# Performance work log

Measured on AMD Instinct MI355X. Metric: run time of the kernel, lower is better.

## Reference

```python
import jax, jax.numpy as jnp
import numpy as np

E = 512        # embed_dim
H = 16         # num_heads
R = 8          # num_relation_heads
NH = H - R     # num_normal_heads
HD = E // H    # head_dim
SCALING = HD ** -0.5
B, LQ, LK = 2, 2048, 2048


def setup_inputs() -> dict:
    key = jax.random.key(0)
    ks = jax.random.split(key, 14)
    s = 1.0 / np.sqrt(E)  # keep pre-softmax logits moderate so exp() is stable
    inp = {
        "query": jax.random.normal(ks[0], (B, LQ, E), jnp.float32),
        "key": jax.random.normal(ks[1], (B, LK, E), jnp.float32),
        "value": jax.random.normal(ks[2], (B, LK, E), jnp.float32),
        "relation_weights": jax.random.uniform(ks[3], (B, R, LQ, LK), jnp.float32),
        "Wq": jax.random.normal(ks[4], (E, E), jnp.float32) * s,
        "bq": jnp.zeros((E,), jnp.float32),
        "Wk": jax.random.normal(ks[5], (E, E), jnp.float32) * s,
        "bk": jnp.zeros((E,), jnp.float32),
        "Wv": jax.random.normal(ks[6], (E, E), jnp.float32) * s,
        "bv": jnp.zeros((E,), jnp.float32),
        "Wo": jax.random.normal(ks[7], (E, E), jnp.float32) * s,
        "bo": jnp.zeros((E,), jnp.float32),
        "ln_gamma": jnp.ones((E,), jnp.float32),
        "ln_beta": jnp.zeros((E,), jnp.float32),
    }
    return inp


def reference(query, key, value, relation_weights, Wq, bq, Wk, bk, Wv, bv, Wo, bo, ln_gamma, ln_beta):
    b, lq, _ = query.shape
    lk = key.shape[1]
    # projections; weights stored as [in, out] so y = x @ W + b
    q = (query @ Wq + bq).reshape(b, lq, H, HD)
    k = (key @ Wk + bk).reshape(b, lk, H, HD)
    v = (value @ Wv + bv).reshape(b, lk, H, HD)
    # scores: [B, H, Lq, Lk]
    scores = jnp.einsum("bqhd,bkhd->bhqk", q, k) * SCALING
    # normal heads: standard softmax
    normal_attn = jax.nn.softmax(scores[:, :NH], axis=-1)
    # relation heads: exp(scores) * relation_weights, renormalized
    rel = jnp.exp(scores[:, NH:]) * relation_weights
    rel = rel / (rel.sum(axis=-1, keepdims=True) + 1e-6)
    attn = jnp.concatenate([normal_attn, rel], axis=1)  # [B, H, Lq, Lk]
    # weighted values -> [B, Lq, E]
    out = jnp.einsum("bhqk,bkhd->bqhd", attn, v).reshape(b, lq, E)
    out = out @ Wo + bo
    # LayerNorm (eps=1e-5, torch default)
    mu = out.mean(axis=-1, keepdims=True)
    var = out.var(axis=-1, keepdims=True)
    out = (out - mu) * jax.lax.rsqrt(var + 1e-5) * ln_gamma + ln_beta
    return out
```

## Files before the change

kernel.cpp:

```cpp
#include <hip/hip_runtime.h>


using u16 = unsigned short;
using u32 = unsigned int;

typedef __attribute__((ext_vector_type(8))) short bf16x8;
typedef __attribute__((ext_vector_type(4))) float f32x4;

#define H_  16
#define NH_ 8
#define HD_ 32
#define L_  2048
#define E_  512
#define B_  2
#define M_  4096
#define KSPLIT 2
static constexpr float SCALE_ = 0.1767766952966369f;

__device__ inline u16 f2bf(float x) {
  union { float f; u32 u; } v; v.f = x;
  u32 r = v.u + 0x7FFFu + ((v.u >> 16) & 1u);
  return (u16)(r >> 16);
}
__device__ inline float bf2f(u16 x) {
  union { u32 u; float f; } v; v.u = ((u32)x) << 16; return v.f;
}
__device__ inline u16 f2h(float x) {
  union { _Float16 h; u16 u; } v; v.h = (_Float16)x; return v.u;
}
__device__ inline float h2f(u16 x) {
  union { u16 u; _Float16 h; } v; v.u = x; return (float)v.h;
}

__global__ __launch_bounds__(256) void k_cvt3(const float* __restrict__ a, const float* __restrict__ b,
                                              const float* __restrict__ c,
                                              u16* __restrict__ oa, u16* __restrict__ ob, u16* __restrict__ oc) {
  int w = blockIdx.y;
  const float* s = (w == 0) ? a : (w == 1) ? b : c;
  u16* d = (w == 0) ? oa : (w == 1) ? ob : oc;
  size_t i = ((size_t)blockIdx.x * 256 + threadIdx.x) * 4;
  float4 v = *(const float4*)(s + i);
  uint2 pk;
  pk.x = (u32)f2bf(v.x) | ((u32)f2bf(v.y) << 16);
  pk.y = (u32)f2bf(v.z) | ((u32)f2bf(v.w) << 16);
  *(uint2*)(d + i) = pk;
}

__global__ __launch_bounds__(256) void k_wtrans(const float* __restrict__ Wq, const float* __restrict__ Wk,
                                                const float* __restrict__ Wv, const float* __restrict__ Wo,
                                                u16* __restrict__ Tq, u16* __restrict__ Tk,
                                                u16* __restrict__ Tv, u16* __restrict__ To) {
  int z = blockIdx.z;
  const float* W = (z == 0) ? Wq : (z == 1) ? Wk : (z == 2) ? Wv : Wo;
  u16* T = (z == 0) ? Tq : (z == 1) ? Tk : (z == 2) ? Tv : To;
  __shared__ u16 tile[64][65];
  int r0 = blockIdx.y * 64, c0 = blockIdx.x * 64;
  int tw = threadIdx.x >> 6, tl = threadIdx.x & 63;
#pragma unroll
  for (int i = 0; i < 16; ++i) {
    int r = i * 4 + tw;
    tile[r][tl] = f2bf(W[(size_t)(r0 + r) * E_ + c0 + tl]);
  }
  __syncthreads();
#pragma unroll
  for (int i = 0; i < 16; ++i) {
    int r = i * 4 + tw;
    T[(size_t)(c0 + r) * E_ + r0 + tl] = tile[tl][r];
  }
}

template <int MODE>
__device__ inline void gemm_body(const u16* __restrict__ A, const u16* __restrict__ Bt,
                                 const float* __restrict__ bias, void* __restrict__ out) {
  __shared__ __align__(16) u16 smem[2 * 128 * 72];
  u16* As = smem;
  u16* Bs = smem + 128 * 72;
  const int tid = threadIdx.x;
  const int lane = tid & 63, wid = tid >> 6;
  const int m0 = blockIdx.x * 128, n0 = blockIdx.y * 128;
  const int wm = (wid >> 1) * 64, wn = (wid & 1) * 64;
  const int mrow = lane & 15, quad = lane >> 4;
  f32x4 acc[4][4] = {};
  for (int k0 = 0; k0 < 512; k0 += 64) {
    __syncthreads();
#pragma unroll
    for (int i = 0; i < 4; ++i) {
      int task = i * 256 + tid;
      int r = task >> 3, c = task & 7;
      *(uint4*)(As + r * 72 + c * 8) = *(const uint4*)(A + (size_t)(m0 + r) * 512 + k0 + c * 8);
      *(uint4*)(Bs + r * 72 + c * 8) = *(const uint4*)(Bt + (size_t)(n0 + r) * 512 + k0 + c * 8);
    }
    __syncthreads();
#pragma unroll
    for (int kk = 0; kk < 64; kk += 32) {
      bf16x8 af[4], bfr[4];
#pragma unroll
      for (int f = 0; f < 4; ++f)
        af[f] = *(const bf16x8*)(As + (wm + f * 16 + mrow) * 72 + kk + quad * 8);
#pragma unroll
      for (int f = 0; f < 4; ++f)
        bfr[f] = *(const bf16x8*)(Bs + (wn + f * 16 + mrow) * 72 + kk + quad * 8);
#pragma unroll
      for (int fm = 0; fm < 4; ++fm)
#pragma unroll
        for (int fn = 0; fn < 4; ++fn)
          acc[fm][fn] = __builtin_amdgcn_mfma_f32_16x16x32_bf16(af[fm], bfr[fn], acc[fm][fn], 0, 0, 0);
    }
  }
  if (MODE == 0) {
    __syncthreads();
    u16* wscr = smem + wid * (64 * 72);
#pragma unroll
    for (int fn = 0; fn < 4; ++fn) {
      float bv = bias[n0 + wn + fn * 16 + mrow];
#pragma unroll
      for (int fm = 0; fm < 4; ++fm)
#pragma unroll
        for (int r = 0; r < 4; ++r)
          wscr[(fm * 16 + quad * 4 + r) * 72 + fn * 16 + mrow] = f2bf(acc[fm][fn][r] + bv);
    }
    asm volatile("s_waitcnt lgkmcnt(0)" ::: "memory");
    const int hg0 = (n0 + wn) >> 5;
#pragma unroll
    for (int c = 0; c < 8; ++c) {
      int linear = c * 64 + lane;
      int hh = linear >> 8;
      int rem = linear & 255;
      int lm = rem >> 2, j = rem & 3;
      uint4 vv = *(const uint4*)(wscr + lm * 72 + hh * 32 + j * 8);
      int gm = m0 + wm + lm;
      int bb = gm >> 11, q = gm & (L_ - 1);
      *(uint4*)((u16*)out + (((size_t)(bb * H_ + hg0 + hh)) * L_ + q) * HD_ + j * 8) = vv;
    }
  } else {
#pragma unroll
    for (int fn = 0; fn < 4; ++fn) {
      int gn = n0 + wn + fn * 16 + mrow;
      float bv = bias[gn];
#pragma unroll
      for (int fm = 0; fm < 4; ++fm)
#pragma unroll
        for (int r = 0; r < 4; ++r) {
          int gm = m0 + wm + fm * 16 + quad * 4 + r;
          ((float*)out)[(size_t)gm * E_ + gn] = acc[fm][fn][r] + bv;
        }
    }
  }
}

__global__ __launch_bounds__(256) void k_gemm_qkv(const u16* Xq, const u16* Xk, const u16* Xv,
                                                  const u16* Tq, const u16* Tk, const u16* Tv,
                                                  const float* bq, const float* bk, const float* bv,
                                                  u16* Qb, u16* Kb, u16* Vb) {
  int z = blockIdx.z;
  const u16* A = (z == 0) ? Xq : (z == 1) ? Xk : Xv;
  const u16* T = (z == 0) ? Tq : (z == 1) ? Tk : Tv;
  const float* bi = (z == 0) ? bq : (z == 1) ? bk : bv;
  u16* o = (z == 0) ? Qb : (z == 1) ? Kb : Vb;
  gemm_body<0>(A, T, bi, o);
}

__global__ __launch_bounds__(256) void k_gemm_o(const u16* A, const u16* T, const float* bi, float* Y) {
  gemm_body<1>(A, T, bi, Y);
}

__global__ __launch_bounds__(256) void k_attn(const u16* __restrict__ Qb, const u16* __restrict__ Kb,
                                              const u16* __restrict__ Vb, const float* __restrict__ relw,
                                              u16* __restrict__ Pnum, float* __restrict__ Pden) {
  const int tid = threadIdx.x, lane = tid & 63, wid = tid >> 6;
  const int q0 = blockIdx.x * 64;
  const int h = blockIdx.y;
  const int b = blockIdx.z & (B_ - 1), s = blockIdx.z >> 1;
  const int kbase = s * (L_ / KSPLIT);
  const bool isrel = (h >= NH_);
  const size_t headOff = ((size_t)(b * H_ + h)) * L_ * HD_;
  const float* wbase = isrel ? relw + ((size_t)(b * (H_ - NH_) + (h - NH_))) * L_ * L_ : nullptr;

  __shared__ __align__(16) u16 Qs[64 * 40];
  __shared__ __align__(16) u16 Ks[64 * 40];
  __shared__ __align__(16) u16 Vts[32 * 72];
  __shared__ __align__(16) u16 Ps[4][16 * 72];
  __shared__ __align__(16) u16 Ws[64 * 68];

  {
    int r = tid >> 2, c = tid & 3;
    *(uint4*)(Qs + r * 40 + c * 8) = *(const uint4*)(Qb + headOff + (size_t)(q0 + r) * HD_ + c * 8);
  }
  __syncthreads();
  const int mrow = lane & 15, quad = lane >> 4;
  bf16x8 qa = *(const bf16x8*)(Qs + (wid * 16 + mrow) * 40 + quad * 8);
  f32x4 accd[2] = {};
  float den[4] = {0.f, 0.f, 0.f, 0.f};

  for (int kt = kbase; kt < kbase + L_ / KSPLIT; kt += 64) {
    __syncthreads();
    if (tid < 128) {
      int p = tid >> 2, c = tid & 3;
      const u16* vsrc = Vb + headOff + (size_t)(kt + 2 * p) * HD_ + c * 8;
      uint4 v0 = *(const uint4*)(vsrc);
      uint4 v1 = *(const uint4*)(vsrc + HD_);
      const u16* s0 = (const u16*)&v0;
      const u16* s1 = (const u16*)&v1;
#pragma unroll
      for (int i = 0; i < 8; ++i) {
        u32 pk = (u32)s0[i] | ((u32)s1[i] << 16);
        *(u32*)(Vts + (c * 8 + i) * 72 + 2 * p) = pk;
      }
    } else {
      int t2 = tid - 128;
#pragma unroll
      for (int i = 0; i < 2; ++i) {
        int task = t2 * 2 + i;
        int r = task >> 2, c = task & 3;
        *(uint4*)(Ks + r * 40 + c * 8) = *(const uint4*)(Kb + headOff + (size_t)(kt + r) * HD_ + c * 8);
      }
    }
    if (isrel) {
      int q = tid >> 2, kc = (tid & 3) * 4;
      const float* wsrc = wbase + (size_t)(q0 + q) * L_ + kt + kc;
#pragma unroll
      for (int j = 0; j < 4; ++j) {
        float4 w4 = *(const float4*)(wsrc + j * 16);
        uint2 pk;
        pk.x = (u32)f2bf(w4.x) | ((u32)f2bf(w4.y) << 16);
        pk.y = (u32)f2bf(w4.z) | ((u32)f2bf(w4.w) << 16);
        *(uint2*)(Ws + q * 68 + kc + j * 16) = pk;
      }
    }
    __syncthreads();

    u16* pw = Ps[wid];
#pragma unroll
    for (int f = 0; f < 4; ++f) {
      bf16x8 kb = *(const bf16x8*)(Ks + (f * 16 + mrow) * 40 + quad * 8);
      f32x4 z = {0.f, 0.f, 0.f, 0.f};
      f32x4 sc = __builtin_amdgcn_mfma_f32_16x16x32_bf16(qa, kb, z, 0, 0, 0);
#pragma unroll
      for (int r = 0; r < 4; ++r) {
        float e = __expf(sc[r] * SCALE_);
        if (isrel)
          e *= bf2f(Ws[(wid * 16 + quad * 4 + r) * 68 + f * 16 + mrow]);
        den[r] += e;
        pw[(quad * 4 + r) * 72 + f * 16 + mrow] = f2bf(e);
      }
    }
    asm volatile("s_waitcnt lgkmcnt(0)" ::: "memory");
#pragma unroll
    for (int kk = 0; kk < 2; ++kk) {
      bf16x8 pa = *(const bf16x8*)(pw + mrow * 72 + kk * 32 + quad * 8);
#pragma unroll
      for (int dh = 0; dh < 2; ++dh) {
        bf16x8 vbf = *(const bf16x8*)(Vts + (dh * 16 + mrow) * 72 + kk * 32 + quad * 8);
        accd[dh] = __builtin_amdgcn_mfma_f32_16x16x32_bf16(pa, vbf, accd[dh], 0, 0, 0);
      }
    }
  }

#pragma unroll
  for (int off = 1; off < 16; off <<= 1)
#pragma unroll
    for (int r = 0; r < 4; ++r) den[r] += __shfl_xor(den[r], off, 64);

  const size_t pidx = ((size_t)(s * B_ + b) * H_ + h) * L_;
#pragma unroll
  for (int dh = 0; dh < 2; ++dh)
#pragma unroll
    for (int r = 0; r < 4; ++r) {
      int qg = q0 + wid * 16 + quad * 4 + r;
      Pnum[(pidx + qg) * HD_ + dh * 16 + mrow] = f2h(accd[dh][r]);
    }
  if (mrow == 0) {
    int qg = q0 + wid * 16 + quad * 4;
    float4 dv = {den[0], den[1], den[2], den[3]};
    *(float4*)(Pden + pidx + qg) = dv;
  }
}

__global__ __launch_bounds__(256) void k_combine(const u16* __restrict__ Pnum, const float* __restrict__ Pden,
                                                 u16* __restrict__ AO) {
  int row = blockIdx.x;
  int tid = threadIdx.x;
  int b = row >> 11, q = row & (L_ - 1);
  int e0 = tid * 2;
  int h = e0 >> 5, d = e0 & (HD_ - 1);
  size_t i0 = ((size_t)(0 * B_ + b) * H_ + h) * L_ + q;
  size_t i1 = ((size_t)(1 * B_ + b) * H_ + h) * L_ + q;
  u32 n0 = *(const u32*)(Pnum + i0 * HD_ + d);
  u32 n1 = *(const u32*)(Pnum + i1 * HD_ + d);
  float den = Pden[i0] + Pden[i1] + ((h >= NH_) ? 1e-6f : 0.f);
  float rinv = 1.0f / den;
  float x = (h2f((u16)n0) + h2f((u16)n1)) * rinv;
  float y = (h2f((u16)(n0 >> 16)) + h2f((u16)(n1 >> 16))) * rinv;
  u32 pk = (u32)f2bf(x) | ((u32)f2bf(y) << 16);
  *(u32*)(AO + (size_t)row * E_ + e0) = pk;
}

__global__ __launch_bounds__(256) void k_ln(const float* __restrict__ Y, const float* __restrict__ gamma,
                                            const float* __restrict__ beta, float* __restrict__ out) {
  int row = blockIdx.x, tid = threadIdx.x;
  const float* y = Y + (size_t)row * E_;
  float2 v = *(const float2*)(y + tid * 2);
  float s = v.x + v.y, sq = v.x * v.x + v.y * v.y;
#pragma unroll
  for (int off = 1; off < 64; off <<= 1) {
    s += __shfl_xor(s, off, 64);
    sq += __shfl_xor(sq, off, 64);
  }
  __shared__ float ss[4], ssq[4];
  int wid = tid >> 6, lane = tid & 63;
  if (lane == 0) { ss[wid] = s; ssq[wid] = sq; }
  __syncthreads();
  s = ss[0] + ss[1] + ss[2] + ss[3];
  sq = ssq[0] + ssq[1] + ssq[2] + ssq[3];
  float mean = s * (1.f / E_);
  float var = sq * (1.f / E_) - mean * mean;
  float rstd = rsqrtf(var + 1e-5f);
  float2 g = *(const float2*)(gamma + tid * 2);
  float2 be = *(const float2*)(beta + tid * 2);
  float2 o;
  o.x = (v.x - mean) * rstd * g.x + be.x;
  o.y = (v.y - mean) * rstd * g.y + be.y;
  *(float2*)(out + (size_t)row * E_ + tid * 2) = o;
}

extern "C" void kernel_launch(void* const* d_in, const int* in_sizes, int n_in,
                              void* d_out, int out_size, void* d_ws, size_t ws_size,
                              hipStream_t stream) {
  const float* query = (const float*)d_in[0];
  const float* key   = (const float*)d_in[1];
  const float* value = (const float*)d_in[2];
  const float* relw  = (const float*)d_in[3];
  const float* Wq = (const float*)d_in[4];
  const float* bq = (const float*)d_in[5];
  const float* Wk = (const float*)d_in[6];
  const float* bk = (const float*)d_in[7];
  const float* Wv = (const float*)d_in[8];
  const float* bv = (const float*)d_in[9];
  const float* Wo = (const float*)d_in[10];
  const float* bo = (const float*)d_in[11];
  const float* gamma = (const float*)d_in[12];
  const float* beta  = (const float*)d_in[13];

  char* ws = (char*)d_ws;
  u16* Xq = (u16*)(ws + 0);
  u16* Xk = (u16*)(ws + 4194304);
  u16* Xv = (u16*)(ws + 8388608);
  u16* Tq = (u16*)(ws + 12582912);
  u16* Tk = (u16*)(ws + 13107200);
  u16* Tv = (u16*)(ws + 13631488);
  u16* To = (u16*)(ws + 14155776);
  u16* Qb = (u16*)(ws + 14680064);
  u16* Kb = (u16*)(ws + 18874368);
  u16* Vb = (u16*)(ws + 23068672);
  u16* AO = (u16*)(ws + 27262976);
  u16*   Pnum = (u16*)(ws + 0);
  float* Pden = (float*)(ws + 8388608);
  float* Y = (float*)(ws + 0);

  k_cvt3<<<dim3(2048, 3, 1), 256, 0, stream>>>(query, key, value, Xq, Xk, Xv);
  k_wtrans<<<dim3(8, 8, 4), 256, 0, stream>>>(Wq, Wk, Wv, Wo, Tq, Tk, Tv, To);
  k_gemm_qkv<<<dim3(32, 4, 3), 256, 0, stream>>>(Xq, Xk, Xv, Tq, Tk, Tv, bq, bk, bv, Qb, Kb, Vb);
  k_attn<<<dim3(32, 16, B_ * KSPLIT), 256, 0, stream>>>(Qb, Kb, Vb, relw, Pnum, Pden);
  k_combine<<<M_, 256, 0, stream>>>(Pnum, Pden, AO);
  k_gemm_o<<<dim3(32, 4, 1), 256, 0, stream>>>(AO, To, bo, Y);
  k_ln<<<M_, 256, 0, stream>>>(Y, gamma, beta, (float*)d_out);
}
```

Before: 498.3 us.

## Fuse prep kernels and combine into GEMM, prefetch attention tiles, use fp16 PV

The input conversion and weight transpose become one launch, and the split-K combine moves into the output GEMM's A-tile load, dropping a kernel and the AO round trip. The attention loop now register-prefetches the next K, V and relation-weight tile while the current one is computed. Softmax scale and log2(e) are folded into Q at projection time so the loop uses exp2. P and V are stored as fp16 and use the f16 MFMA. These cut launches, global traffic and memory latency, at the cost of more registers and possible fp16 range or precision issues.

```diff
diff --git a/kernel.cpp b/kernel.cpp
--- a/kernel.cpp
+++ b/kernel.cpp
@@ -5,6 +5,7 @@
 using u32 = unsigned int;
 
 typedef __attribute__((ext_vector_type(8))) short bf16x8;
+typedef __attribute__((ext_vector_type(8))) _Float16 f16x8;
 typedef __attribute__((ext_vector_type(4))) float f32x4;
 
 #define H_  16
@@ -15,7 +16,7 @@
 #define B_  2
 #define M_  4096
 #define KSPLIT 2
-static constexpr float SCALE_ = 0.1767766952966369f;
+static constexpr float QSCALE_ = 0.17677669529663689f * 1.44269504088896340f;
 
 __device__ inline u16 f2bf(float x) {
   union { float f; u32 u; } v; v.f = x;
@@ -32,29 +33,32 @@
   union { u16 u; _Float16 h; } v; v.u = x; return (float)v.h;
 }
 
-__global__ __launch_bounds__(256) void k_cvt3(const float* __restrict__ a, const float* __restrict__ b,
-                                              const float* __restrict__ c,
-                                              u16* __restrict__ oa, u16* __restrict__ ob, u16* __restrict__ oc) {
-  int w = blockIdx.y;
-  const float* s = (w == 0) ? a : (w == 1) ? b : c;
-  u16* d = (w == 0) ? oa : (w == 1) ? ob : oc;
-  size_t i = ((size_t)blockIdx.x * 256 + threadIdx.x) * 4;
-  float4 v = *(const float4*)(s + i);
-  uint2 pk;
-  pk.x = (u32)f2bf(v.x) | ((u32)f2bf(v.y) << 16);
-  pk.y = (u32)f2bf(v.z) | ((u32)f2bf(v.w) << 16);
-  *(uint2*)(d + i) = pk;
-}
-
-__global__ __launch_bounds__(256) void k_wtrans(const float* __restrict__ Wq, const float* __restrict__ Wk,
-                                                const float* __restrict__ Wv, const float* __restrict__ Wo,
-                                                u16* __restrict__ Tq, u16* __restrict__ Tk,
-                                                u16* __restrict__ Tv, u16* __restrict__ To) {
-  int z = blockIdx.z;
+__global__ __launch_bounds__(256) void k_prep(const float* __restrict__ qa, const float* __restrict__ ka,
+                                              const float* __restrict__ va,
+                                              u16* __restrict__ oq, u16* __restrict__ ok, u16* __restrict__ ov,
+                                              const float* __restrict__ Wq, const float* __restrict__ Wk,
+                                              const float* __restrict__ Wv, const float* __restrict__ Wo,
+                                              u16* __restrict__ Tq, u16* __restrict__ Tk,
+                                              u16* __restrict__ Tv, u16* __restrict__ To) {
+  __shared__ u16 tile[64][65];
+  int y = blockIdx.y;
+  if (y < 3) {
+    const float* s = (y == 0) ? qa : (y == 1) ? ka : va;
+    u16* d = (y == 0) ? oq : (y == 1) ? ok : ov;
+    size_t i = ((size_t)blockIdx.x * 256 + threadIdx.x) * 4;
+    float4 v = *(const float4*)(s + i);
+    uint2 pk;
+    pk.x = (u32)f2bf(v.x) | ((u32)f2bf(v.y) << 16);
+    pk.y = (u32)f2bf(v.z) | ((u32)f2bf(v.w) << 16);
+    *(uint2*)(d + i) = pk;
+    return;
+  }
+  if (blockIdx.x >= 256) return;
+  int bid = blockIdx.x;
+  int z = bid >> 6, rem = bid & 63;
+  int r0 = ((rem >> 3) & 7) * 64, c0 = (rem & 7) * 64;
   const float* W = (z == 0) ? Wq : (z == 1) ? Wk : (z == 2) ? Wv : Wo;
   u16* T = (z == 0) ? Tq : (z == 1) ? Tk : (z == 2) ? Tv : To;
-  __shared__ u16 tile[64][65];
-  int r0 = blockIdx.y * 64, c0 = blockIdx.x * 64;
   int tw = threadIdx.x >> 6, tl = threadIdx.x & 63;
 #pragma unroll
   for (int i = 0; i < 16; ++i) {
@@ -71,7 +75,8 @@
 
 template <int MODE>
 __device__ inline void gemm_body(const u16* __restrict__ A, const u16* __restrict__ Bt,
-                                 const float* __restrict__ bias, void* __restrict__ out) {
+                                 const float* __restrict__ bias, void* __restrict__ out,
+                                 const float* __restrict__ pden, float oscale, int ofmt) {
   __shared__ __align__(16) u16 smem[2 * 128 * 72];
   u16* As = smem;
   u16* Bs = smem + 128 * 72;
@@ -87,8 +92,27 @@
     for (int i = 0; i < 4; ++i) {
       int task = i * 256 + tid;
       int r = task >> 3, c = task & 7;
-      *(uint4*)(As + r * 72 + c * 8) = *(const uint4*)(A + (size_t)(m0 + r) * 512 + k0 + c * 8);
       *(uint4*)(Bs + r * 72 + c * 8) = *(const uint4*)(Bt + (size_t)(n0 + r) * 512 + k0 + c * 8);
+      if (MODE == 0) {
+        *(uint4*)(As + r * 72 + c * 8) = *(const uint4*)(A + (size_t)(m0 + r) * 512 + k0 + c * 8);
+      } else {
+        int gm = m0 + r;
+        int bb = gm >> 11, q = gm & (L_ - 1);
+        int e0 = k0 + c * 8;
+        int hh = e0 >> 5, d = e0 & (HD_ - 1);
+        size_t i0 = ((size_t)(0 * B_ + bb) * H_ + hh) * L_ + q;
+        size_t i1 = ((size_t)(1 * B_ + bb) * H_ + hh) * L_ + q;
+        uint4 n0v = *(const uint4*)(A + i0 * HD_ + d);
+        uint4 n1v = *(const uint4*)(A + i1 * HD_ + d);
+        float den = pden[i0] + pden[i1] + ((hh >= NH_) ? 1e-6f : 0.f);
+        float rinv = __builtin_amdgcn_rcpf(den);
+        const u16* p0 = (const u16*)&n0v;
+        const u16* p1 = (const u16*)&n1v;
+        u16 o8[8];
+#pragma unroll
+        for (int j = 0; j < 8; ++j) o8[j] = f2bf((h2f(p0[j]) + h2f(p1[j])) * rinv);
+        *(uint4*)(As + r * 72 + c * 8) = *(const uint4*)o8;
+      }
     }
     __syncthreads();
 #pragma unroll
@@ -116,8 +140,10 @@
 #pragma unroll
       for (int fm = 0; fm < 4; ++fm)
 #pragma unroll
-        for (int r = 0; r < 4; ++r)
-          wscr[(fm * 16 + quad * 4 + r) * 72 + fn * 16 + mrow] = f2bf(acc[fm][fn][r] + bv);
+        for (int r = 0; r < 4; ++r) {
+          float x = (acc[fm][fn][r] + bv) * oscale;
+          wscr[(fm * 16 + quad * 4 + r) * 72 + fn * 16 + mrow] = ofmt ? f2h(x) : f2bf(x);
+        }
     }
     asm volatile("s_waitcnt lgkmcnt(0)" ::: "memory");
     const int hg0 = (n0 + wn) >> 5;
@@ -157,11 +183,14 @@
   const u16* T = (z == 0) ? Tq : (z == 1) ? Tk : Tv;
   const float* bi = (z == 0) ? bq : (z == 1) ? bk : bv;
   u16* o = (z == 0) ? Qb : (z == 1) ? Kb : Vb;
-  gemm_body<0>(A, T, bi, o);
-}
-
-__global__ __launch_bounds__(256) void k_gemm_o(const u16* A, const u16* T, const float* bi, float* Y) {
-  gemm_body<1>(A, T, bi, Y);
+  float os = (z == 0) ? QSCALE_ : 1.0f;
+  int of = (z == 2) ? 1 : 0;
+  gemm_body<0>(A, T, bi, o, nullptr, os, of);
+}
+
+__global__ __launch_bounds__(256) void k_gemm_o(const u16* Pnum, const u16* T, const float* bi,
+                                                float* Y, const float* Pden) {
+  gemm_body<1>(Pnum, T, bi, Y, Pden, 1.0f, 0);
 }
 
 __global__ __launch_bounds__(256) void k_attn(const u16* __restrict__ Qb, const u16* __restrict__ Kb,
@@ -172,6 +201,7 @@
   const int h = blockIdx.y;
   const int b = blockIdx.z & (B_ - 1), s = blockIdx.z >> 1;
   const int kbase = s * (L_ / KSPLIT);
+  const int kend = kbase + L_ / KSPLIT;
   const bool isrel = (h >= NH_);
   const size_t headOff = ((size_t)(b * H_ + h)) * L_ * HD_;
   const float* wbase = isrel ? relw + ((size_t)(b * (H_ - NH_) + (h - NH_))) * L_ * L_ : nullptr;
@@ -192,41 +222,58 @@
   f32x4 accd[2] = {};
   float den[4] = {0.f, 0.f, 0.f, 0.f};
 
-  for (int kt = kbase; kt < kbase + L_ / KSPLIT; kt += 64) {
-    __syncthreads();
+  uint4 rA, rB;
+  float4 rw[4];
+  const int vp = tid >> 2, vc = tid & 3;
+  const int t2 = tid - 128;
+  const int wq = tid >> 2, wkc = (tid & 3) * 4;
+
+  auto LOAD = [&](int kt) {
     if (tid < 128) {
-      int p = tid >> 2, c = tid & 3;
-      const u16* vsrc = Vb + headOff + (size_t)(kt + 2 * p) * HD_ + c * 8;
-      uint4 v0 = *(const uint4*)(vsrc);
-      uint4 v1 = *(const uint4*)(vsrc + HD_);
-      const u16* s0 = (const u16*)&v0;
-      const u16* s1 = (const u16*)&v1;
+      const u16* vsrc = Vb + headOff + (size_t)(kt + 2 * vp) * HD_ + vc * 8;
+      rA = *(const uint4*)(vsrc);
+      rB = *(const uint4*)(vsrc + HD_);
+    } else {
+      int task0 = t2 * 2, task1 = t2 * 2 + 1;
+      rA = *(const uint4*)(Kb + headOff + (size_t)(kt + (task0 >> 2)) * HD_ + (task0 & 3) * 8);
+      rB = *(const uint4*)(Kb + headOff + (size_t)(kt + (task1 >> 2)) * HD_ + (task1 & 3) * 8);
+    }
+    if (isrel) {
+      const float* wsrc = wbase + (size_t)(q0 + wq) * L_ + kt + wkc;
+#pragma unroll
+      for (int j = 0; j < 4; ++j) rw[j] = *(const float4*)(wsrc + j * 16);
+    }
+  };
+  auto WRITE = [&]() {
+    if (tid < 128) {
+      const u16* s0 = (const u16*)&rA;
+      const u16* s1 = (const u16*)&rB;
 #pragma unroll
       for (int i = 0; i < 8; ++i) {
         u32 pk = (u32)s0[i] | ((u32)s1[i] << 16);
-        *(u32*)(Vts + (c * 8 + i) * 72 + 2 * p) = pk;
+        *(u32*)(Vts + (vc * 8 + i) * 72 + 2 * vp) = pk;
       }
     } else {
-      int t2 = tid - 128;
-#pragma unroll
-      for (int i = 0; i < 2; ++i) {
-        int task = t2 * 2 + i;
-        int r = task >> 2, c = task & 3;
-        *(uint4*)(Ks + r * 40 + c * 8) = *(const uint4*)(Kb + headOff + (size_t)(kt + r) * HD_ + c * 8);
-      }
+      int task0 = t2 * 2, task1 = t2 * 2 + 1;
+      *(uint4*)(Ks + (task0 >> 2) * 40 + (task0 & 3) * 8) = rA;
+      *(uint4*)(Ks + (task1 >> 2) * 40 + (task1 & 3) * 8) = rB;
     }
     if (isrel) {
-      int q = tid >> 2, kc = (tid & 3) * 4;
-      const float* wsrc = wbase + (size_t)(q0 + q) * L_ + kt + kc;
 #pragma unroll
       for (int j = 0; j < 4; ++j) {
-        float4 w4 = *(const float4*)(wsrc + j * 16);
         uint2 pk;
-        pk.x = (u32)f2bf(w4.x) | ((u32)f2bf(w4.y) << 16);
-        pk.y = (u32)f2bf(w4.z) | ((u32)f2bf(w4.w) << 16);
-        *(uint2*)(Ws + q * 68 + kc + j * 16) = pk;
-      }
-    }
+        pk.x = (u32)f2bf(rw[j].x) | ((u32)f2bf(rw[j].y) << 16);
+        pk.y = (u32)f2bf(rw[j].z) | ((u32)f2bf(rw[j].w) << 16);
+        *(uint2*)(Ws + wq * 68 + wkc + j * 16) = pk;
+      }
+    }
+  };
+
+  LOAD(kbase);
+  for (int kt = kbase; kt < kend; kt += 64) {
+    __syncthreads();
+    WRITE();
+    if (kt + 64 < kend) LOAD(kt + 64);
     __syncthreads();
 
     u16* pw = Ps[wid];
@@ -237,21 +284,21 @@
       f32x4 sc = __builtin_amdgcn_mfma_f32_16x16x32_bf16(qa, kb, z, 0, 0, 0);
 #pragma unroll
       for (int r = 0; r < 4; ++r) {
-        float e = __expf(sc[r] * SCALE_);
+        float e = exp2f(sc[r]);
         if (isrel)
           e *= bf2f(Ws[(wid * 16 + quad * 4 + r) * 68 + f * 16 + mrow]);
         den[r] += e;
-        pw[(quad * 4 + r) * 72 + f * 16 + mrow] = f2bf(e);
+        pw[(quad * 4 + r) * 72 + f * 16 + mrow] = f2h(e);
       }
     }
     asm volatile("s_waitcnt lgkmcnt(0)" ::: "memory");
 #pragma unroll
     for (int kk = 0; kk < 2; ++kk) {
-      bf16x8 pa = *(const bf16x8*)(pw + mrow * 72 + kk * 32 + quad * 8);
+      f16x8 pa = *(const f16x8*)(pw + mrow * 72 + kk * 32 + quad * 8);
 #pragma unroll
       for (int dh = 0; dh < 2; ++dh) {
-        bf16x8 vbf = *(const bf16x8*)(Vts + (dh * 16 + mrow) * 72 + kk * 32 + quad * 8);
-        accd[dh] = __builtin_amdgcn_mfma_f32_16x16x32_bf16(pa, vbf, accd[dh], 0, 0, 0);
+        f16x8 vhf = *(const f16x8*)(Vts + (dh * 16 + mrow) * 72 + kk * 32 + quad * 8);
+        accd[dh] = __builtin_amdgcn_mfma_f32_16x16x32_f16(pa, vhf, accd[dh], 0, 0, 0);
       }
     }
   }
@@ -274,25 +321,6 @@
     float4 dv = {den[0], den[1], den[2], den[3]};
     *(float4*)(Pden + pidx + qg) = dv;
   }
-}
-
-__global__ __launch_bounds__(256) void k_combine(const u16* __restrict__ Pnum, const float* __restrict__ Pden,
-                                                 u16* __restrict__ AO) {
-  int row = blockIdx.x;
-  int tid = threadIdx.x;
-  int b = row >> 11, q = row & (L_ - 1);
-  int e0 = tid * 2;
-  int h = e0 >> 5, d = e0 & (HD_ - 1);
-  size_t i0 = ((size_t)(0 * B_ + b) * H_ + h) * L_ + q;
-  size_t i1 = ((size_t)(1 * B_ + b) * H_ + h) * L_ + q;
-  u32 n0 = *(const u32*)(Pnum + i0 * HD_ + d);
-  u32 n1 = *(const u32*)(Pnum + i1 * HD_ + d);
-  float den = Pden[i0] + Pden[i1] + ((h >= NH_) ? 1e-6f : 0.f);
-  float rinv = 1.0f / den;
-  float x = (h2f((u16)n0) + h2f((u16)n1)) * rinv;
-  float y = (h2f((u16)(n0 >> 16)) + h2f((u16)(n1 >> 16))) * rinv;
-  u32 pk = (u32)f2bf(x) | ((u32)f2bf(y) << 16);
-  *(u32*)(AO + (size_t)row * E_ + e0) = pk;
 }
 
 __global__ __launch_bounds__(256) void k_ln(const float* __restrict__ Y, const float* __restrict__ gamma,
@@ -352,16 +380,14 @@
   u16* Qb = (u16*)(ws + 14680064);
   u16* Kb = (u16*)(ws + 18874368);
   u16* Vb = (u16*)(ws + 23068672);
-  u16* AO = (u16*)(ws + 27262976);
   u16*   Pnum = (u16*)(ws + 0);
   float* Pden = (float*)(ws + 8388608);
-  float* Y = (float*)(ws + 0);
-
-  k_cvt3<<<dim3(2048, 3, 1), 256, 0, stream>>>(query, key, value, Xq, Xk, Xv);
-  k_wtrans<<<dim3(8, 8, 4), 256, 0, stream>>>(Wq, Wk, Wv, Wo, Tq, Tk, Tv, To);
+  float* Y = (float*)(ws + 14680064);
+
+  k_prep<<<dim3(2048, 4, 1), 256, 0, stream>>>(query, key, value, Xq, Xk, Xv,
+                                               Wq, Wk, Wv, Wo, Tq, Tk, Tv, To);
   k_gemm_qkv<<<dim3(32, 4, 3), 256, 0, stream>>>(Xq, Xk, Xv, Tq, Tk, Tv, bq, bk, bv, Qb, Kb, Vb);
   k_attn<<<dim3(32, 16, B_ * KSPLIT), 256, 0, stream>>>(Qb, Kb, Vb, relw, Pnum, Pden);
-  k_combine<<<M_, 256, 0, stream>>>(Pnum, Pden, AO);
-  k_gemm_o<<<dim3(32, 4, 1), 256, 0, stream>>>(AO, To, bo, Y);
+  k_gemm_o<<<dim3(32, 4, 1), 256, 0, stream>>>(Pnum, To, bo, Y, Pden);
   k_ln<<<M_, 256, 0, stream>>>(Y, gamma, beta, (float*)d_out);
 }
```

After: 486.3 us. 2.4% less time.
